# Optimization experiments

Measured on AMD Instinct MI355X. Metric: run time of the kernel, lower is better.

## Reference

```python
import jax, jax.numpy as jnp
import numpy as np

N_CLI, N_AGG, E, D, L = 100000, 1000, 1600000, 128, 3


def setup_inputs() -> dict:
    key = jax.random.key(0)
    ks = jax.random.split(key, 16)
    inp = {
        'x_clients': jax.random.normal(ks[0], (N_CLI, D), jnp.float32),
        'x_agg': jax.random.normal(ks[1], (N_AGG, D), jnp.float32),
        'c2a_src': jax.random.randint(ks[2], (E,), 0, N_CLI, jnp.int32),
        'c2a_dst': jax.random.randint(ks[3], (E,), 0, N_AGG, jnp.int32),
        'a2c_src': jax.random.randint(ks[4], (E,), 0, N_AGG, jnp.int32),
        'a2c_dst': jax.random.randint(ks[5], (E,), 0, N_CLI, jnp.int32),
    }
    s = 1.0 / np.sqrt(D)
    # stacked per-layer SAGE params for each edge type: W_l (on aggregated msg), W_r (on dst), b
    inp['Wl_c2a'] = jax.random.uniform(ks[6], (L, D, D), jnp.float32, -s, s)
    inp['Wr_c2a'] = jax.random.uniform(ks[7], (L, D, D), jnp.float32, -s, s)
    inp['b_c2a'] = jax.random.uniform(ks[8], (L, D), jnp.float32, -s, s)
    inp['Wl_a2c'] = jax.random.uniform(ks[9], (L, D, D), jnp.float32, -s, s)
    inp['Wr_a2c'] = jax.random.uniform(ks[10], (L, D, D), jnp.float32, -s, s)
    inp['b_a2c'] = jax.random.uniform(ks[11], (L, D), jnp.float32, -s, s)
    inp['W_lin'] = jax.random.uniform(ks[12], (D, 1), jnp.float32, -s, s)
    inp['b_lin'] = jax.random.uniform(ks[13], (1,), jnp.float32, -s, s)
    return inp


def _sage(x_src, x_dst, src, dst, Wl, Wr, b, n_dst):
    # mean aggregation of gathered source features onto dst nodes
    msg = x_src[src]                                        # [E, D]
    summed = jax.ops.segment_sum(msg, dst, num_segments=n_dst)
    cnt = jax.ops.segment_sum(jnp.ones((src.shape[0], 1), x_src.dtype), dst, num_segments=n_dst)
    mean = summed / jnp.maximum(cnt, 1.0)
    return mean @ Wl + x_dst @ Wr + b


def _leaky(x):
    return jnp.where(x >= 0, x, 0.1 * x)


def reference(x_clients, x_agg, c2a_src, c2a_dst, a2c_src, a2c_dst,
              Wl_c2a, Wr_c2a, b_c2a, Wl_a2c, Wr_a2c, b_a2c, W_lin, b_lin):
    xc, xa = x_clients, x_agg
    for l in range(L):
        new_a = _sage(xc, xa, c2a_src, c2a_dst, Wl_c2a[l], Wr_c2a[l], b_c2a[l], N_AGG)
        new_c = _sage(xa, xc, a2c_src, a2c_dst, Wl_a2c[l], Wr_a2c[l], b_a2c[l], N_CLI)
        xa, xc = _leaky(new_a), _leaky(new_c)
    return (xc @ W_lin + b_lin).squeeze(1)
```

## Files before the change

### kernel.cpp

```cpp
#include <hip/hip_runtime.h>

#define D      128
#define NCLI   100000
#define NAGG   1000
#define NLAYER 3
#define NBKT   782
#define NRNG   8
#define NBIN   (NAGG * NRNG)
#define RMAGIC 343598u
#define NHIST  512
#define NCVTX  (NCLI * D / 4 / 256)
#define NCVTW  ((NLAYER * D * D + 255) / 256)
#define NROWT  (NCLI / 32)

typedef short bf16x8 __attribute__((ext_vector_type(8)));
typedef float f32x16 __attribute__((ext_vector_type(16)));

static __device__ __forceinline__ float leaky(float x) { return x >= 0.f ? x : 0.1f * x; }

static __device__ __forceinline__ unsigned bf16_rn(float f) {
    unsigned u = __float_as_uint(f);
    return (u + 0x7fffu + ((u >> 16) & 1u)) >> 16;
}
static __device__ __forceinline__ float bf_val(unsigned h) { return __uint_as_float(h << 16); }
static __device__ __forceinline__ unsigned pack_bf2(float lo, float hi) {
    return bf16_rn(lo) | (bf16_rn(hi) << 16);
}
static __device__ __forceinline__ float bf_lo(unsigned v) { return __uint_as_float(v << 16); }
static __device__ __forceinline__ float bf_hi(unsigned v) { return __uint_as_float(v & 0xffff0000u); }

__global__ __launch_bounds__(256) void prep(const int* __restrict__ c2a_src,
                                            const int* __restrict__ c2a_dst,
                                            const int* __restrict__ a2c_dst, int E,
                                            int* __restrict__ cnt_ar, int* __restrict__ bcnt,
                                            const float4* __restrict__ X4,
                                            uint2* __restrict__ xhi, uint2* __restrict__ xlo,
                                            const float* __restrict__ W,
                                            unsigned short* __restrict__ Wt) {
    __shared__ int h[NBIN + NBKT];
    int bid = blockIdx.x;
    if (bid < NHIST) {
        for (int i = threadIdx.x; i < NBIN + NBKT; i += 256) h[i] = 0;
        __syncthreads();
        int stride = NHIST * 256;
        for (int e = bid * 256 + threadIdx.x; e < E; e += stride) {
            int s = c2a_src[e];
            int bin = c2a_dst[e] * NRNG + (int)__umulhi((unsigned)s, RMAGIC);
            atomicAdd(&h[bin], 1);
            atomicAdd(&h[NBIN + (a2c_dst[e] >> 7)], 1);
        }
        __syncthreads();
        for (int i = threadIdx.x; i < NBIN; i += 256)
            if (h[i]) atomicAdd(&cnt_ar[i], h[i]);
        for (int i = threadIdx.x; i < NBKT; i += 256)
            if (h[NBIN + i]) atomicAdd(&bcnt[i], h[NBIN + i]);
    } else if (bid < NHIST + NCVTX) {
        int t = (bid - NHIST) * 256 + threadIdx.x;
        float4 f = X4[t];
        unsigned h0 = bf16_rn(f.x), h1 = bf16_rn(f.y), h2 = bf16_rn(f.z), h3 = bf16_rn(f.w);
        xhi[t] = make_uint2(h0 | (h1 << 16), h2 | (h3 << 16));
        xlo[t] = make_uint2(pack_bf2(f.x - bf_val(h0), f.y - bf_val(h1)),
                            pack_bf2(f.z - bf_val(h2), f.w - bf_val(h3)));
    } else {
        int idx = (bid - NHIST - NCVTX) * 256 + threadIdx.x;
        if (idx >= NLAYER * D * D) return;
        int layer = idx >> 14, rem = idx & (D * D - 1);
        int k = rem >> 7, n = rem & 127;
        float w = W[layer * D * D + k * D + n];
        unsigned hh = bf16_rn(w);
        unsigned short* base = Wt + layer * 2 * D * D;
        base[n * D + k] = (unsigned short)hh;
        base[D * D + n * D + k] = (unsigned short)bf16_rn(w - bf_val(hh));
    }
}

__global__ void scan_both(const int* __restrict__ cnt_ar, int* __restrict__ rp_ar,
                          int* __restrict__ cur_ar, const int* __restrict__ bcnt,
                          int* __restrict__ brp, int* __restrict__ bcur) {
    __shared__ int sh[1024];
    int t = threadIdx.x;
    if (blockIdx.x == 0) {
        int v[8];
        int s = 0;
#pragma unroll
        for (int j = 0; j < 8; j++) {
            int idx = t * 8 + j;
            v[j] = (idx < NBIN) ? cnt_ar[idx] : 0;
            s += v[j];
        }
        sh[t] = s;
        __syncthreads();
        for (int off = 1; off < 1024; off <<= 1) {
            int x = (t >= off) ? sh[t - off] : 0;
            __syncthreads();
            sh[t] += x;
            __syncthreads();
        }
        int run = sh[t] - s;
#pragma unroll
        for (int j = 0; j < 8; j++) {
            int idx = t * 8 + j;
            if (idx < NBIN) {
                rp_ar[idx] = run;
                cur_ar[idx] = run;
            }
            run += v[j];
        }
        if (t == 1023) rp_ar[NBIN] = sh[1023];
    } else {
        int v = (t < NBKT) ? bcnt[t] : 0;
        sh[t] = v;
        __syncthreads();
        for (int off = 1; off < 1024; off <<= 1) {
            int x = (t >= off) ? sh[t - off] : 0;
            __syncthreads();
            sh[t] += x;
            __syncthreads();
        }
        if (t == 0) { brp[0] = 0; bcur[0] = 0; }
        if (t < NBKT) {
            brp[t + 1] = sh[t];
            if (t + 1 < NBKT) bcur[t + 1] = sh[t];
        }
    }
}

__global__ __launch_bounds__(1024) void scatter_both(const int* __restrict__ c2a_src,
                                                     const int* __restrict__ c2a_dst,
                                                     const int* __restrict__ a2c_src,
                                                     const int* __restrict__ a2c_dst, int E,
                                                     int* __restrict__ cur_ar,
                                                     int* __restrict__ col_c2a,
                                                     int* __restrict__ bcur,
                                                     int* __restrict__ sorted1) {
    __shared__ int sbuf[2 * NBIN];
    int tid = threadIdx.x;
    if (blockIdx.x < 256) {
        int* h = sbuf;
        int* base = sbuf + NBIN;
        int chunk = (E + 255) / 256;
        int e0 = blockIdx.x * chunk;
        int e1 = min(E, e0 + chunk);
        for (int i = tid; i < NBIN; i += 1024) h[i] = 0;
        __syncthreads();
        for (int e = e0 + tid; e < e1; e += 1024) {
            int s = c2a_src[e];
            atomicAdd(&h[c2a_dst[e] * NRNG + (int)__umulhi((unsigned)s, RMAGIC)], 1);
        }
        __syncthreads();
        for (int i = tid; i < NBIN; i += 1024) {
            int c = h[i];
            base[i] = c ? atomicAdd(&cur_ar[i], c) : 0;
        }
        __syncthreads();
        for (int e = e0 + tid; e < e1; e += 1024) {
            int s = c2a_src[e];
            int bin = c2a_dst[e] * NRNG + (int)__umulhi((unsigned)s, RMAGIC);
            int pos = atomicAdd(&base[bin], 1);
            col_c2a[pos] = s;
        }
    } else {
        int* h = sbuf;
        int* base = sbuf + NBKT;
        int bid = blockIdx.x - 256;
        int chunk = (E + 255) / 256;
        int e0 = bid * chunk;
        int e1 = min(E, e0 + chunk);
        for (int i = tid; i < NBKT; i += 1024) h[i] = 0;
        __syncthreads();
        for (int e = e0 + tid; e < e1; e += 1024) atomicAdd(&h[a2c_dst[e] >> 7], 1);
        __syncthreads();
        for (int i = tid; i < NBKT; i += 1024) {
            int c = h[i];
            base[i] = c ? atomicAdd(&bcur[i], c) : 0;
        }
        __syncthreads();
        for (int e = e0 + tid; e < e1; e += 1024) {
            int d = a2c_dst[e];
            int pos = atomicAdd(&base[d >> 7], 1);
            sorted1[pos] = ((d & 127) << 10) | a2c_src[e];
        }
    }
}

__global__ __launch_bounds__(512) void bucket_csr(const int* __restrict__ brp,
                                                  const int* __restrict__ sorted1,
                                                  int* __restrict__ rp_c,
                                                  int* __restrict__ col) {
    __shared__ int h[128], cur[128];
    int b = blockIdx.x, tid = threadIdx.x;
    if (tid < 128) h[tid] = 0;
    __syncthreads();
    int beg = brp[b], end = brp[b + 1];
    for (int e = beg + tid; e < end; e += 512) atomicAdd(&h[sorted1[e] >> 10], 1);
    __syncthreads();
    if (tid < 128) cur[tid] = h[tid];
    __syncthreads();
    for (int off = 1; off < 128; off <<= 1) {
        int x = 0;
        if (tid < 128 && tid >= off) x = cur[tid - off];
        __syncthreads();
        if (tid < 128) cur[tid] += x;
        __syncthreads();
    }
    if (tid < 128) {
        int start = beg + cur[tid] - h[tid];
        int c = b * 128 + tid;
        if (c < NCLI) rp_c[c] = start;
        cur[tid] = start;
    }
    if (b == NBKT - 1 && tid == 0) rp_c[NCLI] = end;
    __syncthreads();
    for (int e = beg + tid; e < end; e += 512) {
        int p = sorted1[e];
        int pos = atomicAdd(&cur[p >> 10], 1);
        col[pos] = p & 1023;
    }
}


__global__ __launch_bounds__(512) void gather_mean(const unsigned* __restrict__ tbl,
                                                   const int* __restrict__ rp_ar,
                                                   const int* __restrict__ col,
                                                   float* __restrict__ psum) {
    __shared__ float part[4][8][D];
    int quad = blockIdx.x >> 3, r = blockIdx.x & 7;
    int tid = threadIdx.x;
    int a = tid >> 7;
    int sub = (tid >> 4) & 7;
    int sl = tid & 15;
    const uint4* tbl4 = (const uint4*)tbl;
    int agg = quad * 4 + a;
    int bin = agg * NRNG + r;
    int beg = rp_ar[bin], end = rp_ar[bin + 1];
    float f0 = 0, f1 = 0, f2 = 0, f3 = 0, f4 = 0, f5 = 0, f6 = 0, f7 = 0;
    int e = beg + sub;
    for (; e + 8 < end; e += 16) {
        int s0 = col[e];
        int s1 = col[e + 8];
        uint4 v0 = tbl4[(s0 << 4) + sl];
        uint4 v1 = tbl4[(s1 << 4) + sl];
        f0 += bf_lo(v0.x); f1 += bf_hi(v0.x); f2 += bf_lo(v0.y); f3 += bf_hi(v0.y);
        f4 += bf_lo(v0.z); f5 += bf_hi(v0.z); f6 += bf_lo(v0.w); f7 += bf_hi(v0.w);
        f0 += bf_lo(v1.x); f1 += bf_hi(v1.x); f2 += bf_lo(v1.y); f3 += bf_hi(v1.y);
        f4 += bf_lo(v1.z); f5 += bf_hi(v1.z); f6 += bf_lo(v1.w); f7 += bf_hi(v1.w);
    }
    if (e < end) {
        int s0 = col[e];
        uint4 v0 = tbl4[(s0 << 4) + sl];
        f0 += bf_lo(v0.x); f1 += bf_hi(v0.x); f2 += bf_lo(v0.y); f3 += bf_hi(v0.y);
        f4 += bf_lo(v0.z); f5 += bf_hi(v0.z); f6 += bf_lo(v0.w); f7 += bf_hi(v0.w);
    }
    float* pr = &part[a][sub][sl * 8];
    pr[0] = f0; pr[1] = f1; pr[2] = f2; pr[3] = f3;
    pr[4] = f4; pr[5] = f5; pr[6] = f6; pr[7] = f7;
    __syncthreads();
    int c = tid & 127;
    float s = 0.f;
#pragma unroll
    for (int g = 0; g < 8; g++) s += part[a][g][c];
    psum[((size_t)agg * NRNG + r) * D + c] = s;
}

__global__ __launch_bounds__(128) void combine_agg(const float* __restrict__ psum,
                                                   const int* __restrict__ rp_ar,
                                                   const float* xa_old,
                                                   const float* __restrict__ Wl_a2c,
                                                   const float* __restrict__ Wl_c2a,
                                                   const float* __restrict__ Wr_c2a,
                                                   const float* __restrict__ b_c2a,
                                                   unsigned short* __restrict__ ya_bf,
                                                   float* xa_out) {
    __shared__ float mr[D], xr[D];
    int i = blockIdx.x, j = threadIdx.x;
    const float* pr = psum + (size_t)i * NRNG * D + j;
    float s = 0.f;
#pragma unroll
    for (int r = 0; r < NRNG; r++) s += pr[r * D];
    int deg = rp_ar[i * NRNG + NRNG] - rp_ar[i * NRNG];
    mr[j] = s / fmaxf((float)deg, 1.f);
    xr[j] = xa_old[i * D + j];
    __syncthreads();
    float accy = 0.f, accn = b_c2a[j];
#pragma unroll 4
    for (int k = 0; k < D; k++) {
        accy += xr[k] * Wl_a2c[k * D + j];
        accn += mr[k] * Wl_c2a[k * D + j] + xr[k] * Wr_c2a[k * D + j];
    }
    ya_bf[i * D + j] = (unsigned short)bf16_rn(accy);
    xa_out[i * D + j] = leaky(accn);
}

template <int LAST>
__global__ __launch_bounds__(256) void gemm_agg(const unsigned short* __restrict__ Ahi,
                                                const unsigned short* __restrict__ Alo,
                                                const unsigned short* __restrict__ Wt,
                                                const float* __restrict__ bias,
                                                const unsigned* __restrict__ ya,
                                                const int* __restrict__ rowptr,
                                                const int* __restrict__ col,
                                                unsigned* __restrict__ xhi,
                                                unsigned* __restrict__ xlo,
                                                const float* __restrict__ Wlin,
                                                const float* __restrict__ blin,
                                                float* __restrict__ out, int E) {
    __shared__ float smem[32][D];
    int tid = threadIdx.x;
    int wave = tid >> 6, lane = tid & 63;
    int cl = lane & 31, kh = lane >> 5;
    int n0 = wave * 32;
    const unsigned short* Wlo_ = Wt + D * D;
    const unsigned short* wbh = Wt + (size_t)(n0 + cl) * D + kh * 8;
    const unsigned short* wbl = Wlo_ + (size_t)(n0 + cl) * D + kh * 8;
    bf16x8 bhi[8], blo[8];
#pragma unroll
    for (int kc = 0; kc < 8; kc++) {
        bhi[kc] = *(const bf16x8*)(wbh + kc * 16);
        blo[kc] = *(const bf16x8*)(wbl + kc * 16);
    }
    float bv = bias[n0 + cl];
    int m0 = blockIdx.x * 32;
    {
        const unsigned short* ar = Ahi + (size_t)(m0 + cl) * D + kh * 8;
        const unsigned short* al = Alo + (size_t)(m0 + cl) * D + kh * 8;
        bf16x8 ahi[8], alo[8];
#pragma unroll
        for (int kc = 0; kc < 8; kc++) {
            ahi[kc] = *(const bf16x8*)(ar + kc * 16);
            alo[kc] = *(const bf16x8*)(al + kc * 16);
        }
        f32x16 acc;
#pragma unroll
        for (int q = 0; q < 16; q++) acc[q] = bv;
#pragma unroll
        for (int kc = 0; kc < 8; kc++) {
            acc = __builtin_amdgcn_mfma_f32_32x32x16_bf16(ahi[kc], bhi[kc], acc, 0, 0, 0);
            acc = __builtin_amdgcn_mfma_f32_32x32x16_bf16(alo[kc], bhi[kc], acc, 0, 0, 0);
            acc = __builtin_amdgcn_mfma_f32_32x32x16_bf16(ahi[kc], blo[kc], acc, 0, 0, 0);
        }
#pragma unroll
        for (int reg = 0; reg < 16; reg++) {
            int row = (reg & 3) + 8 * (reg >> 2) + 4 * kh;
            smem[row][n0 + cl] = acc[reg];
        }
    }
    __syncthreads();
    const uint4* ya4 = (const uint4*)ya;
    int g = lane >> 4, q = lane & 15;
#pragma unroll
    for (int pass = 0; pass < 2; pass++) {
        int c_local = wave * 8 + pass * 4 + g;
        int gid = m0 + c_local;
        int beg = rowptr[gid], end = rowptr[gid + 1];
        float s0 = 0, s1 = 0, s2 = 0, s3 = 0, s4 = 0, s5 = 0, s6 = 0, s7 = 0;
        for (int ch = beg; ch < end; ch += 16) {
            int len = min(16, end - ch);
            int ec = col[min(ch + q, E - 1)];
            int j = 0;
            for (; j + 8 <= len; j += 8) {
                int r0 = __shfl(ec, j + 0, 16), r1 = __shfl(ec, j + 1, 16);
                int r2 = __shfl(ec, j + 2, 16), r3 = __shfl(ec, j + 3, 16);
                int r4 = __shfl(ec, j + 4, 16), r5 = __shfl(ec, j + 5, 16);
                int r6 = __shfl(ec, j + 6, 16), r7 = __shfl(ec, j + 7, 16);
                uint4 v0 = ya4[(r0 << 4) + q];
                uint4 v1 = ya4[(r1 << 4) + q];
                uint4 v2 = ya4[(r2 << 4) + q];
                uint4 v3 = ya4[(r3 << 4) + q];
                uint4 v4 = ya4[(r4 << 4) + q];
                uint4 v5 = ya4[(r5 << 4) + q];
                uint4 v6 = ya4[(r6 << 4) + q];
                uint4 v7 = ya4[(r7 << 4) + q];
                s0 += bf_lo(v0.x); s1 += bf_hi(v0.x); s2 += bf_lo(v0.y); s3 += bf_hi(v0.y);
                s4 += bf_lo(v0.z); s5 += bf_hi(v0.z); s6 += bf_lo(v0.w); s7 += bf_hi(v0.w);
                s0 += bf_lo(v1.x); s1 += bf_hi(v1.x); s2 += bf_lo(v1.y); s3 += bf_hi(v1.y);
                s4 += bf_lo(v1.z); s5 += bf_hi(v1.z); s6 += bf_lo(v1.w); s7 += bf_hi(v1.w);
                s0 += bf_lo(v2.x); s1 += bf_hi(v2.x); s2 += bf_lo(v2.y); s3 += bf_hi(v2.y);
                s4 += bf_lo(v2.z); s5 += bf_hi(v2.z); s6 += bf_lo(v2.w); s7 += bf_hi(v2.w);
                s0 += bf_lo(v3.x); s1 += bf_hi(v3.x); s2 += bf_lo(v3.y); s3 += bf_hi(v3.y);
                s4 += bf_lo(v3.z); s5 += bf_hi(v3.z); s6 += bf_lo(v3.w); s7 += bf_hi(v3.w);
                s0 += bf_lo(v4.x); s1 += bf_hi(v4.x); s2 += bf_lo(v4.y); s3 += bf_hi(v4.y);
                s4 += bf_lo(v4.z); s5 += bf_hi(v4.z); s6 += bf_lo(v4.w); s7 += bf_hi(v4.w);
                s0 += bf_lo(v5.x); s1 += bf_hi(v5.x); s2 += bf_lo(v5.y); s3 += bf_hi(v5.y);
                s4 += bf_lo(v5.z); s5 += bf_hi(v5.z); s6 += bf_lo(v5.w); s7 += bf_hi(v5.w);
                s0 += bf_lo(v6.x); s1 += bf_hi(v6.x); s2 += bf_lo(v6.y); s3 += bf_hi(v6.y);
                s4 += bf_lo(v6.z); s5 += bf_hi(v6.z); s6 += bf_lo(v6.w); s7 += bf_hi(v6.w);
                s0 += bf_lo(v7.x); s1 += bf_hi(v7.x); s2 += bf_lo(v7.y); s3 += bf_hi(v7.y);
                s4 += bf_lo(v7.z); s5 += bf_hi(v7.z); s6 += bf_lo(v7.w); s7 += bf_hi(v7.w);
            }
            for (; j < len; j++) {
                int rr = __shfl(ec, j, 16);
                uint4 v = ya4[(rr << 4) + q];
                s0 += bf_lo(v.x); s1 += bf_hi(v.x); s2 += bf_lo(v.y); s3 += bf_hi(v.y);
                s4 += bf_lo(v.z); s5 += bf_hi(v.z); s6 += bf_lo(v.w); s7 += bf_hi(v.w);
            }
        }
        float inv = 1.f / fmaxf((float)(end - beg), 1.f);
        float4 y0 = *(const float4*)&smem[c_local][8 * q];
        float4 y1 = *(const float4*)&smem[c_local][8 * q + 4];
        float r0 = leaky(y0.x + s0 * inv);
        float r1 = leaky(y0.y + s1 * inv);
        float r2 = leaky(y0.z + s2 * inv);
        float r3 = leaky(y0.w + s3 * inv);
        float r4 = leaky(y1.x + s4 * inv);
        float r5 = leaky(y1.y + s5 * inv);
        float r6 = leaky(y1.z + s6 * inv);
        float r7 = leaky(y1.w + s7 * inv);
        if (LAST) {
            float4 w0 = *(const float4*)&Wlin[8 * q];
            float4 w1 = *(const float4*)&Wlin[8 * q + 4];
            float v = r0 * w0.x + r1 * w0.y + r2 * w0.z + r3 * w0.w +
                      r4 * w1.x + r5 * w1.y + r6 * w1.z + r7 * w1.w;
#pragma unroll
            for (int off = 8; off > 0; off >>= 1) v += __shfl_down(v, off, 16);
            if (q == 0) out[gid] = v + blin[0];
        } else {
            unsigned h0 = bf16_rn(r0), h1 = bf16_rn(r1), h2 = bf16_rn(r2), h3 = bf16_rn(r3);
            unsigned h4 = bf16_rn(r4), h5 = bf16_rn(r5), h6 = bf16_rn(r6), h7 = bf16_rn(r7);
            uint4 hi, lo;
            hi.x = h0 | (h1 << 16); hi.y = h2 | (h3 << 16);
            hi.z = h4 | (h5 << 16); hi.w = h6 | (h7 << 16);
            lo.x = pack_bf2(r0 - bf_val(h0), r1 - bf_val(h1));
            lo.y = pack_bf2(r2 - bf_val(h2), r3 - bf_val(h3));
            lo.z = pack_bf2(r4 - bf_val(h4), r5 - bf_val(h5));
            lo.w = pack_bf2(r6 - bf_val(h6), r7 - bf_val(h7));
            ((uint4*)xhi)[(gid << 4) + q] = hi;
            ((uint4*)xlo)[(gid << 4) + q] = lo;
        }
    }
}

extern "C" void kernel_launch(void* const* d_in, const int* in_sizes, int n_in,
                              void* d_out, int out_size, void* d_ws, size_t ws_size,
                              hipStream_t stream) {
    const float* x_clients = (const float*)d_in[0];
    const float* x_agg     = (const float*)d_in[1];
    const int*   c2a_src   = (const int*)d_in[2];
    const int*   c2a_dst   = (const int*)d_in[3];
    const int*   a2c_src   = (const int*)d_in[4];
    const int*   a2c_dst   = (const int*)d_in[5];
    const float* Wl_c2a    = (const float*)d_in[6];
    const float* Wr_c2a    = (const float*)d_in[7];
    const float* b_c2a     = (const float*)d_in[8];
    const float* Wl_a2c    = (const float*)d_in[9];
    const float* Wr_a2c    = (const float*)d_in[10];
    const float* b_a2c     = (const float*)d_in[11];
    const float* W_lin     = (const float*)d_in[12];
    const float* b_lin     = (const float*)d_in[13];
    float* out = (float*)d_out;
    const int E = in_sizes[2];

    char* p = (char*)d_ws;
    auto alloc = [&](size_t bytes) {
        char* r = p;
        p += (bytes + 255) & ~(size_t)255;
        return r;
    };
    float*    Yb    = (float*)alloc(sizeof(float) * NCLI * D);
    unsigned* xc_hi = (unsigned*)alloc(sizeof(unsigned) * NCLI * 64);
    unsigned* xc_lo = (unsigned*)alloc(sizeof(unsigned) * NCLI * 64);
    float*    xa    = (float*)alloc(sizeof(float) * NAGG * D);
    unsigned short* ya_bf = (unsigned short*)alloc(sizeof(unsigned short) * NAGG * D);
    unsigned short* Wt = (unsigned short*)alloc(sizeof(unsigned short) * NLAYER * 2 * D * D);
    float* psum  = (float*)alloc(sizeof(float) * NAGG * NRNG * D);
    int* cnt_ar = (int*)alloc(sizeof(int) * (NBIN + NBKT));
    int* bcnt  = cnt_ar + NBIN;
    int* rp_ar = (int*)alloc(sizeof(int) * (NBIN + 1));
    int* cur_ar = (int*)alloc(sizeof(int) * NBIN);
    int* brp   = (int*)alloc(sizeof(int) * (NBKT + 1));
    int* bcur  = (int*)alloc(sizeof(int) * NBKT);
    int* rp_c  = (int*)alloc(sizeof(int) * (NCLI + 1));
    int* col_c2a = (int*)alloc(sizeof(int) * E);
    int* col_a2c = (int*)alloc(sizeof(int) * E);
    int* sorted1 = (int*)Yb;

    hipMemsetAsync(cnt_ar, 0, sizeof(int) * (NBIN + NBKT), stream);

    prep<<<NHIST + NCVTX + NCVTW, 256, 0, stream>>>(c2a_src, c2a_dst, a2c_dst, E, cnt_ar, bcnt,
                                                    (const float4*)x_clients,
                                                    (uint2*)xc_hi, (uint2*)xc_lo,
                                                    Wr_a2c, Wt);
    scan_both<<<2, 1024, 0, stream>>>(cnt_ar, rp_ar, cur_ar, bcnt, brp, bcur);
    scatter_both<<<512, 1024, 0, stream>>>(c2a_src, c2a_dst, a2c_src, a2c_dst, E,
                                           cur_ar, col_c2a, bcur, sorted1);
    bucket_csr<<<NBKT, 512, 0, stream>>>(brp, sorted1, rp_c, col_a2c);

    const float* xa_old = x_agg;
    for (int l = 0; l < NLAYER; l++) {
        gather_mean<<<(NAGG / 4) * NRNG, 512, 0, stream>>>(xc_hi, rp_ar, col_c2a, psum);
        combine_agg<<<NAGG, 128, 0, stream>>>(psum, rp_ar, xa_old,
                                              Wl_a2c + l * D * D, Wl_c2a + l * D * D,
                                              Wr_c2a + l * D * D, b_c2a + l * D, ya_bf, xa);
        if (l < NLAYER - 1) {
            gemm_agg<0><<<NROWT, 256, 0, stream>>>(
                (const unsigned short*)xc_hi, (const unsigned short*)xc_lo,
                Wt + l * 2 * D * D, b_a2c + l * D, (const unsigned*)ya_bf, rp_c, col_a2c,
                xc_hi, xc_lo, nullptr, nullptr, nullptr, E);
        } else {
            gemm_agg<1><<<NROWT, 256, 0, stream>>>(
                (const unsigned short*)xc_hi, (const unsigned short*)xc_lo,
                Wt + l * 2 * D * D, b_a2c + l * D, (const unsigned*)ya_bf, rp_c, col_a2c,
                nullptr, nullptr, W_lin, b_lin, out, E);
        }
        xa_old = xa;
    }
}
```

Measured before the change: 626.1 us.

## Replace a2c edge gather with dense count-matrix MFMA against transposed agg features

Each client tile now builds a dense 32x1008 byte count matrix in LDS with LDS atomics over its incoming a2c edges. It then multiplies that matrix by the transposed bf16 aggregator projection with MFMA, in place of gathering one ya row per edge from global memory. combine_agg writes ya transposed and zero-padded to 1008 columns to feed the MFMA B operand. This trades irregular per-edge global loads for a fixed 63-step MFMA loop plus about 32KB of LDS per block. The risks are lower occupancy, and 8-bit counts that overflow if a client-aggregator pair has more than 255 edges.

```diff
diff --git a/kernel.cpp b/kernel.cpp
--- a/kernel.cpp
+++ b/kernel.cpp
@@ -12,6 +12,8 @@
 #define NCVTX  (NCLI * D / 4 / 256)
 #define NCVTW  ((NLAYER * D * D + 255) / 256)
 #define NROWT  (NCLI / 32)
+#define KAGG   1008
+#define CSTRIDE 1008
 
 typedef short bf16x8 __attribute__((ext_vector_type(8)));
 typedef float f32x16 __attribute__((ext_vector_type(16)));
@@ -269,7 +271,7 @@
                                                    const float* __restrict__ Wl_c2a,
                                                    const float* __restrict__ Wr_c2a,
                                                    const float* __restrict__ b_c2a,
-                                                   unsigned short* __restrict__ ya_bf,
+                                                   unsigned short* __restrict__ yaT,
                                                    float* xa_out) {
     __shared__ float mr[D], xr[D];
     int i = blockIdx.x, j = threadIdx.x;
@@ -287,7 +289,7 @@
         accy += xr[k] * Wl_a2c[k * D + j];
         accn += mr[k] * Wl_c2a[k * D + j] + xr[k] * Wr_c2a[k * D + j];
     }
-    ya_bf[i * D + j] = (unsigned short)bf16_rn(accy);
+    yaT[(size_t)j * KAGG + i] = (unsigned short)bf16_rn(accy);
     xa_out[i * D + j] = leaky(accn);
 }
 
@@ -296,7 +298,7 @@
                                                 const unsigned short* __restrict__ Alo,
                                                 const unsigned short* __restrict__ Wt,
                                                 const float* __restrict__ bias,
-                                                const unsigned* __restrict__ ya,
+                                                const unsigned short* __restrict__ yaT,
                                                 const int* __restrict__ rowptr,
                                                 const int* __restrict__ col,
                                                 unsigned* __restrict__ xhi,
@@ -304,107 +306,93 @@
                                                 const float* __restrict__ Wlin,
                                                 const float* __restrict__ blin,
                                                 float* __restrict__ out, int E) {
-    __shared__ float smem[32][D];
+    __shared__ __attribute__((aligned(16))) unsigned char lds_raw[32 * CSTRIDE];
+    __shared__ float invd[32];
+    (void)E;
     int tid = threadIdx.x;
     int wave = tid >> 6, lane = tid & 63;
     int cl = lane & 31, kh = lane >> 5;
     int n0 = wave * 32;
-    const unsigned short* Wlo_ = Wt + D * D;
-    const unsigned short* wbh = Wt + (size_t)(n0 + cl) * D + kh * 8;
-    const unsigned short* wbl = Wlo_ + (size_t)(n0 + cl) * D + kh * 8;
-    bf16x8 bhi[8], blo[8];
-#pragma unroll
-    for (int kc = 0; kc < 8; kc++) {
-        bhi[kc] = *(const bf16x8*)(wbh + kc * 16);
-        blo[kc] = *(const bf16x8*)(wbl + kc * 16);
+    int m0 = blockIdx.x * 32;
+    unsigned* cnt32 = (unsigned*)lds_raw;
+    uint4* z4 = (uint4*)lds_raw;
+    for (int i = tid; i < 32 * CSTRIDE / 16; i += 256) z4[i] = make_uint4(0, 0, 0, 0);
+    if (tid < 32) {
+        int dg = rowptr[m0 + tid + 1] - rowptr[m0 + tid];
+        invd[tid] = 1.f / fmaxf((float)dg, 1.f);
+    }
+    __syncthreads();
+    int g16 = tid >> 4, q16 = tid & 15;
+#pragma unroll
+    for (int cc = 0; cc < 2; cc++) {
+        int c_local = g16 * 2 + cc;
+        int beg = rowptr[m0 + c_local], end = rowptr[m0 + c_local + 1];
+        for (int e = beg + q16; e < end; e += 16) {
+            int idx = c_local * CSTRIDE + col[e];
+            atomicAdd(&cnt32[idx >> 2], 1u << ((idx & 3) * 8));
+        }
     }
     float bv = bias[n0 + cl];
-    int m0 = blockIdx.x * 32;
+    f32x16 acc1;
+#pragma unroll
+    for (int qq = 0; qq < 16; qq++) acc1[qq] = bv;
     {
+        const unsigned short* Wlo_ = Wt + D * D;
         const unsigned short* ar = Ahi + (size_t)(m0 + cl) * D + kh * 8;
         const unsigned short* al = Alo + (size_t)(m0 + cl) * D + kh * 8;
-        bf16x8 ahi[8], alo[8];
+        const unsigned short* wh = Wt + (size_t)(n0 + cl) * D + kh * 8;
+        const unsigned short* wl = Wlo_ + (size_t)(n0 + cl) * D + kh * 8;
 #pragma unroll
         for (int kc = 0; kc < 8; kc++) {
-            ahi[kc] = *(const bf16x8*)(ar + kc * 16);
-            alo[kc] = *(const bf16x8*)(al + kc * 16);
-        }
-        f32x16 acc;
-#pragma unroll
-        for (int q = 0; q < 16; q++) acc[q] = bv;
-#pragma unroll
-        for (int kc = 0; kc < 8; kc++) {
-            acc = __builtin_amdgcn_mfma_f32_32x32x16_bf16(ahi[kc], bhi[kc], acc, 0, 0, 0);
-            acc = __builtin_amdgcn_mfma_f32_32x32x16_bf16(alo[kc], bhi[kc], acc, 0, 0, 0);
-            acc = __builtin_amdgcn_mfma_f32_32x32x16_bf16(ahi[kc], blo[kc], acc, 0, 0, 0);
-        }
-#pragma unroll
-        for (int reg = 0; reg < 16; reg++) {
-            int row = (reg & 3) + 8 * (reg >> 2) + 4 * kh;
-            smem[row][n0 + cl] = acc[reg];
-        }
-    }
-    __syncthreads();
-    const uint4* ya4 = (const uint4*)ya;
+            bf16x8 ahi = *(const bf16x8*)(ar + kc * 16);
+            bf16x8 alo = *(const bf16x8*)(al + kc * 16);
+            bf16x8 bh = *(const bf16x8*)(wh + kc * 16);
+            bf16x8 bl = *(const bf16x8*)(wl + kc * 16);
+            acc1 = __builtin_amdgcn_mfma_f32_32x32x16_bf16(ahi, bh, acc1, 0, 0, 0);
+            acc1 = __builtin_amdgcn_mfma_f32_32x32x16_bf16(alo, bh, acc1, 0, 0, 0);
+            acc1 = __builtin_amdgcn_mfma_f32_32x32x16_bf16(ahi, bl, acc1, 0, 0, 0);
+        }
+    }
+    __syncthreads();
+    f32x16 acc2;
+#pragma unroll
+    for (int qq = 0; qq < 16; qq++) acc2[qq] = 0.f;
+    {
+        const unsigned char* crow = lds_raw + cl * CSTRIDE + kh * 8;
+        const unsigned short* brow = yaT + (size_t)(n0 + cl) * KAGG + kh * 8;
+        for (int s = 0; s < KAGG / 16; s++) {
+            uint2 cw = *(const uint2*)(crow + s * 16);
+            unsigned w0 = cw.x, w1 = cw.y;
+            float f0 = (float)(w0 & 255), f1 = (float)((w0 >> 8) & 255);
+            float f2 = (float)((w0 >> 16) & 255), f3 = (float)(w0 >> 24);
+            float f4 = (float)(w1 & 255), f5 = (float)((w1 >> 8) & 255);
+            float f6 = (float)((w1 >> 16) & 255), f7 = (float)(w1 >> 24);
+            union { unsigned u[4]; bf16x8 v; } af;
+            af.u[0] = (__float_as_uint(f0) >> 16) | (__float_as_uint(f1) & 0xffff0000u);
+            af.u[1] = (__float_as_uint(f2) >> 16) | (__float_as_uint(f3) & 0xffff0000u);
+            af.u[2] = (__float_as_uint(f4) >> 16) | (__float_as_uint(f5) & 0xffff0000u);
+            af.u[3] = (__float_as_uint(f6) >> 16) | (__float_as_uint(f7) & 0xffff0000u);
+            bf16x8 bfrag = *(const bf16x8*)(brow + s * 16);
+            acc2 = __builtin_amdgcn_mfma_f32_32x32x16_bf16(af.v, bfrag, acc2, 0, 0, 0);
+        }
+    }
+    __syncthreads();
+    float (*smem)[D] = (float(*)[D])lds_raw;
+#pragma unroll
+    for (int reg = 0; reg < 16; reg++) {
+        int row = (reg & 3) + 8 * (reg >> 2) + 4 * kh;
+        smem[row][n0 + cl] = leaky(acc1[reg] + acc2[reg] * invd[row]);
+    }
+    __syncthreads();
     int g = lane >> 4, q = lane & 15;
 #pragma unroll
     for (int pass = 0; pass < 2; pass++) {
         int c_local = wave * 8 + pass * 4 + g;
         int gid = m0 + c_local;
-        int beg = rowptr[gid], end = rowptr[gid + 1];
-        float s0 = 0, s1 = 0, s2 = 0, s3 = 0, s4 = 0, s5 = 0, s6 = 0, s7 = 0;
-        for (int ch = beg; ch < end; ch += 16) {
-            int len = min(16, end - ch);
-            int ec = col[min(ch + q, E - 1)];
-            int j = 0;
-            for (; j + 8 <= len; j += 8) {
-                int r0 = __shfl(ec, j + 0, 16), r1 = __shfl(ec, j + 1, 16);
-                int r2 = __shfl(ec, j + 2, 16), r3 = __shfl(ec, j + 3, 16);
-                int r4 = __shfl(ec, j + 4, 16), r5 = __shfl(ec, j + 5, 16);
-                int r6 = __shfl(ec, j + 6, 16), r7 = __shfl(ec, j + 7, 16);
-                uint4 v0 = ya4[(r0 << 4) + q];
-                uint4 v1 = ya4[(r1 << 4) + q];
-                uint4 v2 = ya4[(r2 << 4) + q];
-                uint4 v3 = ya4[(r3 << 4) + q];
-                uint4 v4 = ya4[(r4 << 4) + q];
-                uint4 v5 = ya4[(r5 << 4) + q];
-                uint4 v6 = ya4[(r6 << 4) + q];
-                uint4 v7 = ya4[(r7 << 4) + q];
-                s0 += bf_lo(v0.x); s1 += bf_hi(v0.x); s2 += bf_lo(v0.y); s3 += bf_hi(v0.y);
-                s4 += bf_lo(v0.z); s5 += bf_hi(v0.z); s6 += bf_lo(v0.w); s7 += bf_hi(v0.w);
-                s0 += bf_lo(v1.x); s1 += bf_hi(v1.x); s2 += bf_lo(v1.y); s3 += bf_hi(v1.y);
-                s4 += bf_lo(v1.z); s5 += bf_hi(v1.z); s6 += bf_lo(v1.w); s7 += bf_hi(v1.w);
-                s0 += bf_lo(v2.x); s1 += bf_hi(v2.x); s2 += bf_lo(v2.y); s3 += bf_hi(v2.y);
-                s4 += bf_lo(v2.z); s5 += bf_hi(v2.z); s6 += bf_lo(v2.w); s7 += bf_hi(v2.w);
-                s0 += bf_lo(v3.x); s1 += bf_hi(v3.x); s2 += bf_lo(v3.y); s3 += bf_hi(v3.y);
-                s4 += bf_lo(v3.z); s5 += bf_hi(v3.z); s6 += bf_lo(v3.w); s7 += bf_hi(v3.w);
-                s0 += bf_lo(v4.x); s1 += bf_hi(v4.x); s2 += bf_lo(v4.y); s3 += bf_hi(v4.y);
-                s4 += bf_lo(v4.z); s5 += bf_hi(v4.z); s6 += bf_lo(v4.w); s7 += bf_hi(v4.w);
-                s0 += bf_lo(v5.x); s1 += bf_hi(v5.x); s2 += bf_lo(v5.y); s3 += bf_hi(v5.y);
-                s4 += bf_lo(v5.z); s5 += bf_hi(v5.z); s6 += bf_lo(v5.w); s7 += bf_hi(v5.w);
-                s0 += bf_lo(v6.x); s1 += bf_hi(v6.x); s2 += bf_lo(v6.y); s3 += bf_hi(v6.y);
-                s4 += bf_lo(v6.z); s5 += bf_hi(v6.z); s6 += bf_lo(v6.w); s7 += bf_hi(v6.w);
-                s0 += bf_lo(v7.x); s1 += bf_hi(v7.x); s2 += bf_lo(v7.y); s3 += bf_hi(v7.y);
-                s4 += bf_lo(v7.z); s5 += bf_hi(v7.z); s6 += bf_lo(v7.w); s7 += bf_hi(v7.w);
-            }
-            for (; j < len; j++) {
-                int rr = __shfl(ec, j, 16);
-                uint4 v = ya4[(rr << 4) + q];
-                s0 += bf_lo(v.x); s1 += bf_hi(v.x); s2 += bf_lo(v.y); s3 += bf_hi(v.y);
-                s4 += bf_lo(v.z); s5 += bf_hi(v.z); s6 += bf_lo(v.w); s7 += bf_hi(v.w);
-            }
-        }
-        float inv = 1.f / fmaxf((float)(end - beg), 1.f);
         float4 y0 = *(const float4*)&smem[c_local][8 * q];
         float4 y1 = *(const float4*)&smem[c_local][8 * q + 4];
-        float r0 = leaky(y0.x + s0 * inv);
-        float r1 = leaky(y0.y + s1 * inv);
-        float r2 = leaky(y0.z + s2 * inv);
-        float r3 = leaky(y0.w + s3 * inv);
-        float r4 = leaky(y1.x + s4 * inv);
-        float r5 = leaky(y1.y + s5 * inv);
-        float r6 = leaky(y1.z + s6 * inv);
-        float r7 = leaky(y1.w + s7 * inv);
+        float r0 = y0.x, r1 = y0.y, r2 = y0.z, r3 = y0.w;
+        float r4 = y1.x, r5 = y1.y, r6 = y1.z, r7 = y1.w;
         if (LAST) {
             float4 w0 = *(const float4*)&Wlin[8 * q];
             float4 w1 = *(const float4*)&Wlin[8 * q + 4];
@@ -459,7 +447,7 @@
     unsigned* xc_hi = (unsigned*)alloc(sizeof(unsigned) * NCLI * 64);
     unsigned* xc_lo = (unsigned*)alloc(sizeof(unsigned) * NCLI * 64);
     float*    xa    = (float*)alloc(sizeof(float) * NAGG * D);
-    unsigned short* ya_bf = (unsigned short*)alloc(sizeof(unsigned short) * NAGG * D);
+    unsigned short* yaT = (unsigned short*)alloc(sizeof(unsigned short) * D * KAGG);
     unsigned short* Wt = (unsigned short*)alloc(sizeof(unsigned short) * NLAYER * 2 * D * D);
     float* psum  = (float*)alloc(sizeof(float) * NAGG * NRNG * D);
     int* cnt_ar = (int*)alloc(sizeof(int) * (NBIN + NBKT));
@@ -474,6 +462,7 @@
     int* sorted1 = (int*)Yb;
 
     hipMemsetAsync(cnt_ar, 0, sizeof(int) * (NBIN + NBKT), stream);
+    hipMemsetAsync(yaT, 0, sizeof(unsigned short) * D * KAGG, stream);
 
     prep<<<NHIST + NCVTX + NCVTW, 256, 0, stream>>>(c2a_src, c2a_dst, a2c_dst, E, cnt_ar, bcnt,
                                                     (const float4*)x_clients,
@@ -489,16 +478,16 @@
         gather_mean<<<(NAGG / 4) * NRNG, 512, 0, stream>>>(xc_hi, rp_ar, col_c2a, psum);
         combine_agg<<<NAGG, 128, 0, stream>>>(psum, rp_ar, xa_old,
                                               Wl_a2c + l * D * D, Wl_c2a + l * D * D,
-                                              Wr_c2a + l * D * D, b_c2a + l * D, ya_bf, xa);
+                                              Wr_c2a + l * D * D, b_c2a + l * D, yaT, xa);
         if (l < NLAYER - 1) {
             gemm_agg<0><<<NROWT, 256, 0, stream>>>(
                 (const unsigned short*)xc_hi, (const unsigned short*)xc_lo,
-                Wt + l * 2 * D * D, b_a2c + l * D, (const unsigned*)ya_bf, rp_c, col_a2c,
+                Wt + l * 2 * D * D, b_a2c + l * D, yaT, rp_c, col_a2c,
                 xc_hi, xc_lo, nullptr, nullptr, nullptr, E);
         } else {
             gemm_agg<1><<<NROWT, 256, 0, stream>>>(
                 (const unsigned short*)xc_hi, (const unsigned short*)xc_lo,
-                Wt + l * 2 * D * D, b_a2c + l * D, (const unsigned*)ya_bf, rp_c, col_a2c,
+                Wt + l * 2 * D * D, b_a2c + l * D, yaT, rp_c, col_a2c,
                 nullptr, nullptr, W_lin, b_lin, out, E);
         }
         xa_old = xa;
```

After: 677.7 us. +8.2%, slower.
